# Performance work log

Hardware: AMD Instinct MI355X
Metric: run time of the kernel (lower is better)

## Reference

```python
import jax, jax.numpy as jnp
import numpy as np

NEG_INF = -1e20


def setup_inputs() -> dict:
    key = jax.random.key(0)
    kq, kk, kv, kl = jax.random.split(key, 4)
    B, NQ, NKV, D_QK, D_V = 16, 2048, 2048, 64, 64
    Q_batch = jax.random.normal(kq, (B, NQ, D_QK), dtype=jnp.float32)
    K_batch = jax.random.normal(kk, (B, NKV, D_QK), dtype=jnp.float32)
    V_batch = jax.random.normal(kv, (B, NKV, D_V), dtype=jnp.float32)
    valid_lens = jax.random.randint(kl, (B,), 0, NKV, dtype=jnp.int32)
    return {"Q_batch": Q_batch, "K_batch": K_batch, "V_batch": V_batch,
            "valid_lens": valid_lens}


def reference(Q_batch, K_batch, V_batch, valid_lens):
    d = Q_batch.shape[-1]
    # scores: (B, n_q, n_kv)
    S = jnp.einsum("bqd,bkd->bqk", Q_batch, K_batch) / jnp.sqrt(
        jnp.asarray(d, dtype=Q_batch.dtype))
    n_kv = S.shape[-1]
    # mask kv positions k >= valid_lens[b] (1-D valid_lens broadcast over queries)
    kv_idx = jnp.arange(n_kv)  # (n_kv,)
    mask = kv_idx[None, None, :] < valid_lens[:, None, None]  # (B,1,n_kv)
    S = jnp.where(mask, S, NEG_INF)
    W = jax.nn.softmax(S, axis=-1)
    # dropout rate is 0.0 (eval) -> identity
    return jnp.einsum("bqk,bkv->bqv", W, V_batch)
```

## Files before the change

### kernel.cpp

```cpp
#include <hip/hip_runtime.h>
#include <hip/hip_bf16.h>


typedef __attribute__((ext_vector_type(8))) short short8;
typedef __attribute__((ext_vector_type(4))) short short4v;
typedef __attribute__((ext_vector_type(4))) float float4v;
typedef __attribute__((ext_vector_type(16))) float f32x16;

#define BATCH 16
#define NQ 2048
#define NKV 2048
#define DH 64
#define KVB 64
#define NTILES (NKV / KVB)
#define TILE_ELEMS (KVB * DH)
#define NEG_INF -1e20f
#define SCALE_LOG2 0.180336880111120f

__device__ __forceinline__ short f2bf(float x) {
    union { float f; unsigned u; } v; v.f = x;
    unsigned r = (v.u + 0x7fffu + ((v.u >> 16) & 1u)) >> 16;
    return (short)r;
}

__device__ __forceinline__ short8 cvt8(float4v a, float4v b) {
    short8 r;
    r[0] = f2bf(a[0]); r[1] = f2bf(a[1]); r[2] = f2bf(a[2]); r[3] = f2bf(a[3]);
    r[4] = f2bf(b[0]); r[5] = f2bf(b[1]); r[6] = f2bf(b[2]); r[7] = f2bf(b[3]);
    return r;
}

__device__ __forceinline__ float fexp2(float x) {
    float r; asm("v_exp_f32 %0, %1" : "=v"(r) : "v"(x)); return r;
}

__global__ __launch_bounds__(256) void prep_kernel(
    const float* __restrict__ K, const float* __restrict__ V,
    const int* __restrict__ valid_lens,
    short* __restrict__ Kf, short* __restrict__ Vf)
{
    const int b    = blockIdx.x >> 5;
    const int tile = blockIdx.x & 31;
    const int vlen = valid_lens[b];
    const int nkv  = (vlen == 0) ? NKV : vlen;
    if (tile * KVB >= nkv) return;

    const int tid = threadIdx.x;
    const int ln  = tid & 63;
    const int l31 = ln & 31;
    const int hi8 = (ln >> 5) * 8;
    const size_t gbase = ((size_t)b * NKV + (size_t)tile * KVB) * DH;
    short* kt = Kf + (((size_t)b * NTILES + tile) * TILE_ELEMS);
    short* vt = Vf + (((size_t)b * NTILES + tile) * TILE_ELEMS);

#pragma unroll
    for (int s = 0; s < 2; ++s) {
        const int kk = tid >> 6;
        const int kv = s * 32 + l31;
        const int d  = kk * 16 + hi8;
        const float* p = K + gbase + (size_t)kv * DH + d;
        *reinterpret_cast<short8*>(kt + (s * 256 + tid) * 8) =
            cvt8(*reinterpret_cast<const float4v*>(p),
                 *reinterpret_cast<const float4v*>(p + 4));
    }
    {
        const int kv0 = (tid >> 4) << 2;
        const int d0  = (tid & 15) << 2;
        const float* p = V + gbase + (size_t)kv0 * DH + d0;
        float4v r0 = *reinterpret_cast<const float4v*>(p);
        float4v r1 = *reinterpret_cast<const float4v*>(p + DH);
        float4v r2 = *reinterpret_cast<const float4v*>(p + 2 * DH);
        float4v r3 = *reinterpret_cast<const float4v*>(p + 3 * DH);
        const int ks  = kv0 >> 4;
        const int hiv = (kv0 >> 3) & 1;
        const int j0  = kv0 & 7;
#pragma unroll
        for (int k = 0; k < 4; ++k) {
            const int d    = d0 + k;
            const int lanev = (d & 31) + 32 * hiv;
            short4v w;
            w[0] = f2bf(r0[k]); w[1] = f2bf(r1[k]);
            w[2] = f2bf(r2[k]); w[3] = f2bf(r3[k]);
            *reinterpret_cast<short4v*>(
                vt + (((d >> 5) * 4 + ks) * 64 + lanev) * 8 + j0) = w;
        }
    }
}

__global__ __launch_bounds__(512) void attn_fwd_kernel(
    const float* __restrict__ Q,
    const short* __restrict__ Kf,
    const short* __restrict__ Vf,
    const int* __restrict__ valid_lens,
    float* __restrict__ O)
{
    __shared__ float  mrg[4][2048];
    __shared__ float2 mlb[4][32];

    const int tid  = threadIdx.x;
    const int wave = tid >> 6;
    const int lane = tid & 63;
    const int l31  = lane & 31;
    const int hi   = lane >> 5;
    const int h    = wave >> 2;
    const int qsub = wave & 3;

    const int b  = blockIdx.x & 15;
    const int qt = blockIdx.x >> 4;
    const int qbase = qt * 128 + qsub * 32;

    const int vlen  = valid_lens[b];
    const int nkv   = (vlen == 0) ? NKV : vlen;
    const int tiles = (nkv + KVB - 1) / KVB;
    const int nh = (tiles + 1 - h) >> 1;

    const float* Qb = Q + ((size_t)b * NQ + qbase + l31) * DH;
    short8 qfrag[4];
#pragma unroll
    for (int kk = 0; kk < 4; ++kk) {
        const float* p = Qb + kk * 16 + hi * 8;
        float4v a = *reinterpret_cast<const float4v*>(p);
        float4v c = *reinterpret_cast<const float4v*>(p + 4);
#pragma unroll
        for (int j = 0; j < 4; ++j) { a[j] *= SCALE_LOG2; c[j] *= SCALE_LOG2; }
        qfrag[kk] = cvt8(a, c);
    }

    const short* Kfb = Kf + (size_t)b * NTILES * TILE_ELEMS + lane * 8;
    const short* Vfb = Vf + (size_t)b * NTILES * TILE_ELEMS + lane * 8;

    auto load_k = [&](short8 (&kf)[8], int tile) {
        const short* p = Kfb + (size_t)tile * TILE_ELEMS;
#pragma unroll
        for (int i = 0; i < 8; ++i)
            kf[i] = *reinterpret_cast<const short8*>(p + i * 512);
    };

    f32x16 acc_oA[2], acc_oB[2];
#pragma unroll
    for (int t = 0; t < 2; ++t)
#pragma unroll
        for (int r = 0; r < 16; ++r) { acc_oA[t][r] = 0.f; acc_oB[t][r] = 0.f; }
    float m = -INFINITY, lsum = 0.f;

    short8 kf0[8], kf1[8];

    auto body = [&](short8 (&kc)[8], short8 (&kn)[8], f32x16 (&am)[2], int it) {
        const int tile = 2 * it + h;

        short8 vfr[8];
        {
            const short* p = Vfb + (size_t)tile * TILE_ELEMS;
#pragma unroll
            for (int i = 0; i < 8; ++i)
                vfr[i] = *reinterpret_cast<const short8*>(p + i * 512);
        }

        f32x16 acs[2];
#pragma unroll
        for (int s = 0; s < 2; ++s)
#pragma unroll
            for (int r = 0; r < 16; ++r) acs[s][r] = 0.f;
        __builtin_amdgcn_s_setprio(1);
#pragma unroll
        for (int s = 0; s < 2; ++s)
#pragma unroll
            for (int kk = 0; kk < 4; ++kk)
                acs[s] = __builtin_amdgcn_mfma_f32_32x32x16_bf16(
                    kc[s * 4 + kk], qfrag[kk], acs[s], 0, 0, 0);
        __builtin_amdgcn_s_setprio(0);

        if (it + 1 < nh) load_k(kn, 2 * (it + 1) + h);

        if (vlen < (tile + 1) * KVB) {
            const int kvb0 = tile * KVB + 4 * hi;
#pragma unroll
            for (int s = 0; s < 2; ++s) {
                const int vlim = vlen - (kvb0 + s * 32);
#pragma unroll
                for (int r = 0; r < 16; ++r) {
                    const int rc = (r & 3) + 8 * (r >> 2);
                    acs[s][r] = (rc < vlim) ? acs[s][r] : NEG_INF;
                }
            }
        }

        float mx[8];
#pragma unroll
        for (int r = 0; r < 8; ++r)
            mx[r] = fmaxf(fmaxf(acs[0][r], acs[0][r + 8]),
                          fmaxf(acs[1][r], acs[1][r + 8]));
#pragma unroll
        for (int d = 4; d; d >>= 1)
#pragma unroll
            for (int r = 0; r < d; ++r) mx[r] = fmaxf(mx[r], mx[r + d]);
        float x = mx[0];
        x = fmaxf(x, __shfl_xor(x, 32, 64));

        float mn = m;
        if (!__all(x <= m + 8.f)) {
            mn = fmaxf(m, x);
            const float alpha = fexp2(m - mn);
            m = mn;
            lsum *= alpha;
#pragma unroll
            for (int r = 0; r < 16; ++r) {
                const int rc = (r & 3) + 8 * (r >> 2);
                const float ar = __shfl(alpha, rc + 4 * hi, 64);
                acc_oA[0][r] *= ar; acc_oA[1][r] *= ar;
                acc_oB[0][r] *= ar; acc_oB[1][r] *= ar;
            }
        }

#pragma unroll
        for (int s = 0; s < 2; ++s)
#pragma unroll
            for (int r = 0; r < 16; ++r) acs[s][r] = fexp2(acs[s][r] - mn);
        float sm[8];
#pragma unroll
        for (int r = 0; r < 8; ++r)
            sm[r] = (acs[0][r] + acs[0][r + 8]) + (acs[1][r] + acs[1][r + 8]);
#pragma unroll
        for (int d = 4; d; d >>= 1)
#pragma unroll
            for (int r = 0; r < d; ++r) sm[r] += sm[r + d];
        float rs = sm[0];
        rs += __shfl_xor(rs, 32, 64);
        lsum += rs;

        unsigned pk[2][4][2];
#pragma unroll
        for (int s = 0; s < 2; ++s)
#pragma unroll
            for (int be = 0; be < 4; ++be)
#pragma unroll
                for (int c = 0; c < 2; ++c)
                    asm("v_cvt_pk_bf16_f32 %0, %1, %2"
                        : "=v"(pk[s][be][c])
                        : "v"(acs[s][4 * be + 2 * c]),
                          "v"(acs[s][4 * be + 2 * c + 1]));

        __builtin_amdgcn_s_setprio(1);
#pragma unroll
        for (int ks = 0; ks < 4; ++ks) {
            const int s = ks >> 1, g = ks & 1;
            unsigned w0 = pk[s][2 * g][0], w2 = pk[s][2 * g + 1][0];
            unsigned w1 = pk[s][2 * g][1], w3 = pk[s][2 * g + 1][1];
            asm("v_permlane32_swap_b32 %0, %1" : "+v"(w0), "+v"(w2));
            asm("v_permlane32_swap_b32 %0, %1" : "+v"(w1), "+v"(w3));
            union { unsigned u[4]; short8 s8; } pf;
            pf.u[0] = w0; pf.u[1] = w1; pf.u[2] = w2; pf.u[3] = w3;
#pragma unroll
            for (int t = 0; t < 2; ++t)
                am[t] = __builtin_amdgcn_mfma_f32_32x32x16_bf16(
                    pf.s8, vfr[t * 4 + ks], am[t], 0, 0, 0);
        }
        __builtin_amdgcn_s_setprio(0);
    };

    if (nh > 0) load_k(kf0, h);
    int it = 0;
    for (; it + 1 < nh; it += 2) {
        body(kf0, kf1, acc_oA, it);
        body(kf1, kf0, acc_oB, it + 1);
    }
    if (it < nh) body(kf0, kf1, acc_oA, it);

#pragma unroll
    for (int t = 0; t < 2; ++t)
#pragma unroll
        for (int r = 0; r < 16; ++r) acc_oA[t][r] += acc_oB[t][r];

    if (h == 1) {
#pragma unroll
        for (int t = 0; t < 2; ++t)
#pragma unroll
            for (int r = 0; r < 16; ++r)
                mrg[qsub][(t * 16 + r) * 64 + lane] = acc_oA[t][r];
        if (lane < 32) mlb[qsub][lane] = float2{m, lsum};
    }
    __syncthreads();
    if (h == 0) {
        const float2 o1 = mlb[qsub][l31];
        const float m1 = o1.x, l1 = o1.y;
        const float M  = (l1 > 0.f) ? fmaxf(m, m1) : m;
        const float w0 = fexp2(m - M);
        const float w1 = (l1 > 0.f) ? fexp2(m1 - M) : 0.f;
        const float L  = lsum * w0 + l1 * w1;
        const float a0 = w0 / L, a1 = w1 / L;
        float* Ob = O + ((size_t)b * NQ + qbase) * DH;
#pragma unroll
        for (int r = 0; r < 16; ++r) {
            const int rc = (r & 3) + 8 * (r >> 2);
            const float a0r = __shfl(a0, rc + 4 * hi, 64);
            const float a1r = __shfl(a1, rc + 4 * hi, 64);
#pragma unroll
            for (int t = 0; t < 2; ++t) {
                const float oh = mrg[qsub][(t * 16 + r) * 64 + lane];
                Ob[(size_t)(rc + 4 * hi) * DH + t * 32 + l31] =
                    acc_oA[t][r] * a0r + oh * a1r;
            }
        }
    }
}

extern "C" void kernel_launch(void* const* d_in, const int* in_sizes, int n_in,
                              void* d_out, int out_size, void* d_ws, size_t ws_size,
                              hipStream_t stream) {
    const float* Q = (const float*)d_in[0];
    const float* K = (const float*)d_in[1];
    const float* V = (const float*)d_in[2];
    const int* vl  = (const int*)d_in[3];
    float* Out     = (float*)d_out;

    short* Kws = (short*)d_ws;
    short* Vws = Kws + (size_t)BATCH * NTILES * TILE_ELEMS;

    prep_kernel<<<dim3(BATCH * NTILES), dim3(256), 0, stream>>>(K, V, vl, Kws, Vws);
    attn_fwd_kernel<<<dim3(BATCH * (NQ / 128)), dim3(512), 0, stream>>>(
        Q, Kws, Vws, vl, Out);
}
```

Measured before the change: 35.09 us.

## Software-pipeline QK^T of the next tile ahead of softmax and PV

Splits the loop body into separate QK^T and softmax+PV stages and reorders them so the next tile's score MFMAs are issued before the current tile's softmax and PV work. The aim is to let MFMA work overlap with the exp/reduction VALU work and to give K loads more lead time. In exchange it keeps two score buffers live, which raises VGPR pressure and could lower occupancy or cause spills.

```diff
diff --git a/kernel.cpp b/kernel.cpp
--- a/kernel.cpp
+++ b/kernel.cpp
@@ -129,8 +129,8 @@
     const short* Kfb = Kf + (size_t)b * NTILES * TILE_ELEMS + lane * 8;
     const short* Vfb = Vf + (size_t)b * NTILES * TILE_ELEMS + lane * 8;
 
-    auto load_k = [&](short8 (&kf)[8], int tile) {
-        const short* p = Kfb + (size_t)tile * TILE_ELEMS;
+    auto load_k = [&](short8 (&kf)[8], int k) {
+        const short* p = Kfb + (size_t)(2 * k + h) * TILE_ELEMS;
 #pragma unroll
         for (int i = 0; i < 8; ++i)
             kf[i] = *reinterpret_cast<const short8*>(p + i * 512);
@@ -143,10 +143,26 @@
         for (int r = 0; r < 16; ++r) { acc_oA[t][r] = 0.f; acc_oB[t][r] = 0.f; }
     float m = -INFINITY, lsum = 0.f;
 
-    short8 kf0[8], kf1[8];
-
-    auto body = [&](short8 (&kc)[8], short8 (&kn)[8], f32x16 (&am)[2], int it) {
-        const int tile = 2 * it + h;
+    short8 kfA[8], kfB[8];
+    f32x16 sA[2], sB[2];
+
+    auto qkt = [&](short8 (&kc)[8], f32x16 (&s)[2]) {
+#pragma unroll
+        for (int ss = 0; ss < 2; ++ss)
+#pragma unroll
+            for (int r = 0; r < 16; ++r) s[ss][r] = 0.f;
+        __builtin_amdgcn_s_setprio(1);
+#pragma unroll
+        for (int ss = 0; ss < 2; ++ss)
+#pragma unroll
+            for (int kk = 0; kk < 4; ++kk)
+                s[ss] = __builtin_amdgcn_mfma_f32_32x32x16_bf16(
+                    kc[ss * 4 + kk], qfrag[kk], s[ss], 0, 0, 0);
+        __builtin_amdgcn_s_setprio(0);
+    };
+
+    auto soft_pv = [&](f32x16 (&s)[2], f32x16 (&am)[2], int k) {
+        const int tile = 2 * k + h;
 
         short8 vfr[8];
         {
@@ -156,31 +172,15 @@
                 vfr[i] = *reinterpret_cast<const short8*>(p + i * 512);
         }
 
-        f32x16 acs[2];
-#pragma unroll
-        for (int s = 0; s < 2; ++s)
-#pragma unroll
-            for (int r = 0; r < 16; ++r) acs[s][r] = 0.f;
-        __builtin_amdgcn_s_setprio(1);
-#pragma unroll
-        for (int s = 0; s < 2; ++s)
-#pragma unroll
-            for (int kk = 0; kk < 4; ++kk)
-                acs[s] = __builtin_amdgcn_mfma_f32_32x32x16_bf16(
-                    kc[s * 4 + kk], qfrag[kk], acs[s], 0, 0, 0);
-        __builtin_amdgcn_s_setprio(0);
-
-        if (it + 1 < nh) load_k(kn, 2 * (it + 1) + h);
-
         if (vlen < (tile + 1) * KVB) {
             const int kvb0 = tile * KVB + 4 * hi;
 #pragma unroll
-            for (int s = 0; s < 2; ++s) {
-                const int vlim = vlen - (kvb0 + s * 32);
+            for (int ss = 0; ss < 2; ++ss) {
+                const int vlim = vlen - (kvb0 + ss * 32);
 #pragma unroll
                 for (int r = 0; r < 16; ++r) {
                     const int rc = (r & 3) + 8 * (r >> 2);
-                    acs[s][r] = (rc < vlim) ? acs[s][r] : NEG_INF;
+                    s[ss][r] = (rc < vlim) ? s[ss][r] : NEG_INF;
                 }
             }
         }
@@ -188,18 +188,18 @@
         float mx[8];
 #pragma unroll
         for (int r = 0; r < 8; ++r)
-            mx[r] = fmaxf(fmaxf(acs[0][r], acs[0][r + 8]),
-                          fmaxf(acs[1][r], acs[1][r + 8]));
+            mx[r] = fmaxf(fmaxf(s[0][r], s[0][r + 8]),
+                          fmaxf(s[1][r], s[1][r + 8]));
 #pragma unroll
         for (int d = 4; d; d >>= 1)
 #pragma unroll
             for (int r = 0; r < d; ++r) mx[r] = fmaxf(mx[r], mx[r + d]);
-        float x = mx[0];
-        x = fmaxf(x, __shfl_xor(x, 32, 64));
+        float xv = mx[0];
+        xv = fmaxf(xv, __shfl_xor(xv, 32, 64));
 
         float mn = m;
-        if (!__all(x <= m + 8.f)) {
-            mn = fmaxf(m, x);
+        if (!__all(xv <= m + 8.f)) {
+            mn = fmaxf(m, xv);
             const float alpha = fexp2(m - mn);
             m = mn;
             lsum *= alpha;
@@ -213,13 +213,13 @@
         }
 
 #pragma unroll
-        for (int s = 0; s < 2; ++s)
-#pragma unroll
-            for (int r = 0; r < 16; ++r) acs[s][r] = fexp2(acs[s][r] - mn);
+        for (int ss = 0; ss < 2; ++ss)
+#pragma unroll
+            for (int r = 0; r < 16; ++r) s[ss][r] = fexp2(s[ss][r] - mn);
         float sm[8];
 #pragma unroll
         for (int r = 0; r < 8; ++r)
-            sm[r] = (acs[0][r] + acs[0][r + 8]) + (acs[1][r] + acs[1][r + 8]);
+            sm[r] = (s[0][r] + s[0][r + 8]) + (s[1][r] + s[1][r + 8]);
 #pragma unroll
         for (int d = 4; d; d >>= 1)
 #pragma unroll
@@ -230,22 +230,22 @@
 
         unsigned pk[2][4][2];
 #pragma unroll
-        for (int s = 0; s < 2; ++s)
+        for (int ss = 0; ss < 2; ++ss)
 #pragma unroll
             for (int be = 0; be < 4; ++be)
 #pragma unroll
                 for (int c = 0; c < 2; ++c)
                     asm("v_cvt_pk_bf16_f32 %0, %1, %2"
-                        : "=v"(pk[s][be][c])
-                        : "v"(acs[s][4 * be + 2 * c]),
-                          "v"(acs[s][4 * be + 2 * c + 1]));
+                        : "=v"(pk[ss][be][c])
+                        : "v"(s[ss][4 * be + 2 * c]),
+                          "v"(s[ss][4 * be + 2 * c + 1]));
 
         __builtin_amdgcn_s_setprio(1);
 #pragma unroll
         for (int ks = 0; ks < 4; ++ks) {
-            const int s = ks >> 1, g = ks & 1;
-            unsigned w0 = pk[s][2 * g][0], w2 = pk[s][2 * g + 1][0];
-            unsigned w1 = pk[s][2 * g][1], w3 = pk[s][2 * g + 1][1];
+            const int ss = ks >> 1, g = ks & 1;
+            unsigned w0 = pk[ss][2 * g][0], w2 = pk[ss][2 * g + 1][0];
+            unsigned w1 = pk[ss][2 * g][1], w3 = pk[ss][2 * g + 1][1];
             asm("v_permlane32_swap_b32 %0, %1" : "+v"(w0), "+v"(w2));
             asm("v_permlane32_swap_b32 %0, %1" : "+v"(w1), "+v"(w3));
             union { unsigned u[4]; short8 s8; } pf;
@@ -258,13 +258,20 @@
         __builtin_amdgcn_s_setprio(0);
     };
 
-    if (nh > 0) load_k(kf0, h);
+    if (nh > 0) { load_k(kfA, 0); qkt(kfA, sA); }
+    if (nh > 1) load_k(kfB, 1);
     int it = 0;
     for (; it + 1 < nh; it += 2) {
-        body(kf0, kf1, acc_oA, it);
-        body(kf1, kf0, acc_oB, it + 1);
-    }
-    if (it < nh) body(kf0, kf1, acc_oA, it);
+        qkt(kfB, sB);
+        if (it + 2 < nh) load_k(kfA, it + 2);
+        soft_pv(sA, acc_oA, it);
+        if (it + 2 < nh) {
+            qkt(kfA, sA);
+            if (it + 3 < nh) load_k(kfB, it + 3);
+        }
+        soft_pv(sB, acc_oB, it + 1);
+    }
+    if (it < nh) soft_pv(sA, acc_oA, it);
 
 #pragma unroll
     for (int t = 0; t < 2; ++t)
```

Result: slower. 48.48 us (+38.2%).
